# Optimization experiments

Measured on AMD Instinct MI355X. Metric: run time of the kernel, lower is better.

Reference implementation:

```python
import jax, jax.numpy as jnp
import numpy as np

TEMPERATURE = 0.07
EPS = 1e-8  # F.cosine_similarity eps


def setup_inputs() -> dict:
    key = jax.random.key(0)
    k1, k2, k3, k4 = jax.random.split(key, 4)
    N, D, M, C = 4096, 1024, 8192, 100
    q = jax.random.normal(k1, (N, D), dtype=jnp.float32)
    labels = jax.random.randint(k2, (N,), 0, C, dtype=jnp.int32)
    memory_logits = jax.random.normal(k3, (N, M), dtype=jnp.float32)
    memory_targets = jax.random.bernoulli(k4, 0.5, (N, M)).astype(jnp.float32)
    return {"q": q, "labels": labels, "memory_logits": memory_logits,
            "memory_targets": memory_targets}


def reference(q, labels, memory_logits, memory_targets):
    N = q.shape[0]
    # cosine similarity as normalize + GEMM (second operand detached, as in torch)
    qn = q / jnp.maximum(jnp.linalg.norm(q, axis=-1, keepdims=True), EPS)
    sims = qn @ jax.lax.stop_gradient(qn).T               # [N, N]
    src_contrast = sims / TEMPERATURE
    logits_max = jax.lax.stop_gradient(
        jnp.max(src_contrast, axis=1, keepdims=True))
    src_logits = src_contrast - logits_max                # [N, N]
    # positive-pair mask with self excluded
    src_targets = (labels[:, None] == labels[None, :]).astype(jnp.float32)
    self_mask = 1.0 - jnp.eye(N, dtype=jnp.float32)
    src_targets = src_targets * self_mask
    targets = jnp.concatenate([src_targets, memory_targets], axis=1)  # [N, N+M]
    src_exp_logits = jnp.exp(src_logits) * self_mask
    logits = jnp.concatenate([src_logits, memory_logits], axis=1)     # [N, N+M]
    denom = src_exp_logits.sum(axis=1) + jnp.exp(memory_logits).sum(axis=1)
    log_prob = logits - jnp.log(denom)[:, None]
    mean_log_prob_pos = (targets * log_prob).sum(axis=1) / targets.sum(axis=1)
    return -jnp.mean(mean_log_prob_pos)
```

## Files before the change

### kernel.cpp

```cpp
#include <hip/hip_runtime.h>
#include <hip/hip_bf16.h>
#include <math.h>

typedef unsigned short u16;
typedef __bf16 bf16x8 __attribute__((ext_vector_type(8)));
typedef float f32x4 __attribute__((ext_vector_type(4)));
typedef unsigned short u16x4 __attribute__((ext_vector_type(4)));

#define NROW 4096
#define KDIM 1024
#define MDIM 8192
#define TILE 128
#define BK 64
#define NCT (NROW / TILE)
#define NGEMM (NCT * (NROW / TILE))
#define NMEM  NROW

__device__ __forceinline__ u16 f2bf(float x) {
    unsigned int u = __float_as_uint(x);
    unsigned int r = (u + 0x7fffu + ((u >> 16) & 1u)) >> 16;
    return (u16)r;
}

__device__ __forceinline__ void gload16(const u16* g, u16* l) {
    __builtin_amdgcn_global_load_lds(
        (const __attribute__((address_space(1))) void*)g,
        (__attribute__((address_space(3))) void*)l,
        16, 0, 0);
}

__global__ void k_normalize(const float* __restrict__ q, u16* __restrict__ qn) {
    const int r = blockIdx.x;
    const int t = threadIdx.x;
    const int lane = t & 63, wid = t >> 6;
    const float4* qr = (const float4*)(q + (size_t)r * KDIM);
    float4 v = qr[t];
    float ss = v.x * v.x + v.y * v.y + v.z * v.z + v.w * v.w;
    #pragma unroll
    for (int d = 1; d < 64; d <<= 1) ss += __shfl_xor(ss, d);
    __shared__ float red[4];
    if (lane == 0) red[wid] = ss;
    __syncthreads();
    float tot = red[0] + red[1] + red[2] + red[3];
    float nrm = sqrtf(tot);
    float inv = 1.0f / fmaxf(nrm, 1e-8f);
    u16x4 o;
    o[0] = f2bf(v.x * inv); o[1] = f2bf(v.y * inv);
    o[2] = f2bf(v.z * inv); o[3] = f2bf(v.w * inv);
    *(u16x4*)(qn + (size_t)r * KDIM + t * 4) = o;
}

__global__ void k_fused(const u16* __restrict__ qn, const int* __restrict__ labels,
                        const float* __restrict__ ml, const float* __restrict__ mt,
                        float4* __restrict__ partials, float4* __restrict__ memq) {
    __shared__ u16 ldsA[TILE * BK];
    __shared__ u16 ldsB[TILE * BK];
    __shared__ int labR[TILE], labC[TILE];

    const int bid = blockIdx.x;
    const int t = threadIdx.x;
    const int w = t >> 6, lane = t & 63;
    const int g = bid / 5, rem = bid % 5;

    if (rem != 4) {
        const int r = g * 4 + rem;
        const float4* pl = (const float4*)(ml + (size_t)r * MDIM);
        const float4* pt = (const float4*)(mt + (size_t)r * MDIM);
        const int base = w * 512 + lane;
        float4 L[8], T[8];
        #pragma unroll
        for (int j = 0; j < 8; ++j) L[j] = pl[base + j * 64];
        #pragma unroll
        for (int j = 0; j < 8; ++j) T[j] = pt[base + j * 64];
        float S2 = 0.f, dot = 0.f, smt = 0.f;
        #pragma unroll
        for (int j = 0; j < 8; ++j) {
            S2  += __expf(L[j].x) + __expf(L[j].y) + __expf(L[j].z) + __expf(L[j].w);
            dot += T[j].x * L[j].x + T[j].y * L[j].y + T[j].z * L[j].z + T[j].w * L[j].w;
            smt += T[j].x + T[j].y + T[j].z + T[j].w;
        }
        #pragma unroll
        for (int d = 1; d < 64; d <<= 1) {
            S2  += __shfl_xor(S2, d);
            dot += __shfl_xor(dot, d);
            smt += __shfl_xor(smt, d);
        }
        if (lane == 0) memq[r * 4 + w] = make_float4(S2, dot, smt, 0.f);
        return;
    }

    const int ct = g & 31, bi = g >> 5;
    const int rowbase = bi * TILE, colbase = ct * TILE;

    if (t < 128) labR[t] = labels[rowbase + t];
    else labC[t - 128] = labels[colbase + (t - 128)];

    const int wr = (w >> 1) * 64, wc = (w & 1) * 64;
    const int cl = lane & 15, cg = lane >> 4;

    const int sr = lane >> 3;
    const int skb = lane & 7;

    f32x4 acc[4][4];
    #pragma unroll
    for (int i = 0; i < 4; ++i)
        #pragma unroll
        for (int j = 0; j < 4; ++j)
            acc[i][j] = {0.f, 0.f, 0.f, 0.f};

    for (int ks = 0; ks < KDIM / BK; ++ks) {
        const int k0 = ks * BK;
        #pragma unroll
        for (int it = 0; it < 4; ++it) {
            int c = w * 4 + it;
            int rr = c * 8 + sr;
            const u16* ga = qn + (size_t)(rowbase + rr) * KDIM + k0 + skb * 8;
            gload16(ga, ldsA + c * 512);
            const u16* gb = qn + (size_t)(colbase + rr) * KDIM + k0 + skb * 8;
            gload16(gb, ldsB + c * 512);
        }
        asm volatile("s_waitcnt vmcnt(0)" ::: "memory");
        __syncthreads();
        #pragma unroll
        for (int k2 = 0; k2 < 2; ++k2) {
            bf16x8 a[4], b[4];
            #pragma unroll
            for (int f = 0; f < 4; ++f) {
                a[f] = *(const bf16x8*)&ldsA[(wr + f * 16 + cl) * BK + k2 * 32 + cg * 8];
                b[f] = *(const bf16x8*)&ldsB[(wc + f * 16 + cl) * BK + k2 * 32 + cg * 8];
            }
            #pragma unroll
            for (int fm = 0; fm < 4; ++fm)
                #pragma unroll
                for (int fn = 0; fn < 4; ++fn)
                    acc[fm][fn] = __builtin_amdgcn_mfma_f32_16x16x32_bf16(
                        a[fm], b[fn], acc[fm][fn], 0, 0, 0);
        }
        __syncthreads();
    }

    const float invT = (float)(1.0 / 0.07);
    #pragma unroll
    for (int fm = 0; fm < 4; ++fm) {
        #pragma unroll
        for (int reg = 0; reg < 4; ++reg) {
            const int lr = wr + fm * 16 + cg * 4 + reg;
            const int gi = rowbase + lr;
            const int li = labR[lr];
            float c0 = acc[fm][0][reg] * invT;
            float c1 = acc[fm][1][reg] * invT;
            float c2 = acc[fm][2][reg] * invT;
            float c3 = acc[fm][3][reg] * invT;
            float m = fmaxf(fmaxf(c0, c1), fmaxf(c2, c3));
            #pragma unroll
            for (int d = 1; d < 16; d <<= 1) m = fmaxf(m, __shfl_xor(m, d));
            float se = 0.f, ps = 0.f, cnt = 0.f;
            #pragma unroll
            for (int fn = 0; fn < 4; ++fn) {
                float c = (fn == 0) ? c0 : (fn == 1) ? c1 : (fn == 2) ? c2 : c3;
                const int lc = wc + fn * 16 + cl;
                const int gj = colbase + lc;
                const bool self = (gj == gi);
                se += self ? 0.f : __expf(c - m);
                const bool pos = (!self) && (labC[lc] == li);
                ps += pos ? c : 0.f;
                cnt += pos ? 1.f : 0.f;
            }
            #pragma unroll
            for (int d = 1; d < 16; d <<= 1) {
                se  += __shfl_xor(se, d);
                ps  += __shfl_xor(ps, d);
                cnt += __shfl_xor(cnt, d);
            }
            if (cl == 0) partials[(size_t)ct * NROW + gi] = make_float4(m, se, ps, cnt);
        }
    }
}

__global__ void k_combine(const float4* __restrict__ partials, const float4* __restrict__ memq,
                          float* __restrict__ vals) {
    const int r = blockIdx.x * blockDim.x + threadIdx.x;
    if (r >= NROW) return;
    float M = -3.4e38f;
    #pragma unroll 4
    for (int ct = 0; ct < NCT; ++ct) M = fmaxf(M, partials[(size_t)ct * NROW + r].x);
    float S1 = 0.f, ps = 0.f, cnt = 0.f;
    #pragma unroll 4
    for (int ct = 0; ct < NCT; ++ct) {
        float4 p = partials[(size_t)ct * NROW + r];
        S1 += p.y * __expf(p.x - M);
        ps += p.z;
        cnt += p.w;
    }
    float S2 = 0.f, mdot = 0.f, smt = 0.f;
    #pragma unroll
    for (int k = 0; k < 4; ++k) {
        float4 mq = memq[r * 4 + k];
        S2 += mq.x; mdot += mq.y; smt += mq.z;
    }
    float L = logf(S1 + S2);
    float val = (ps - cnt * (M + L) + mdot - smt * L) / (cnt + smt);
    vals[r] = val;
}

__global__ void k_finalize(const float* __restrict__ vals, float* __restrict__ out) {
    const int t = threadIdx.x;
    const int lane = t & 63, wid = t >> 6;
    float s = 0.f;
    for (int i = t; i < NROW; i += 256) s += vals[i];
    #pragma unroll
    for (int d = 1; d < 64; d <<= 1) s += __shfl_xor(s, d);
    __shared__ float red[4];
    if (lane == 0) red[wid] = s;
    __syncthreads();
    if (t == 0) out[0] = -(red[0] + red[1] + red[2] + red[3]) * (1.0f / (float)NROW);
}

extern "C" void kernel_launch(void* const* d_in, const int* in_sizes, int n_in,
                              void* d_out, int out_size, void* d_ws, size_t ws_size,
                              hipStream_t stream) {
    const float* q  = (const float*)d_in[0];
    const int* labels = (const int*)d_in[1];
    const float* ml = (const float*)d_in[2];
    const float* mt = (const float*)d_in[3];
    float* out = (float*)d_out;

    char* w = (char*)d_ws;
    u16* qn          = (u16*)w;
    float4* partials = (float4*)(w + 8388608);
    float4* memq     = (float4*)(w + 10485760);
    float* vals      = (float*)(w + 10747904);

    k_normalize<<<NROW, 256, 0, stream>>>(q, qn);
    k_fused<<<NGEMM + NMEM, 256, 0, stream>>>(qn, labels, ml, mt, partials, memq);
    k_combine<<<NROW / 256, 256, 0, stream>>>(partials, memq, vals);
    k_finalize<<<1, 256, 0, stream>>>(vals, out);
}
```

Baseline: 123.0 us.

## Stream memory rows per wave via double-buffered LDS loads, interleave 1:1 with GEMM

The memory-logit reduction drops from four blocks per row group to 1024 blocks, with each wave now owning a whole row. Each wave streams its row in 1 KB chunks through double-buffered LDS using global_load_lds. Stream blocks now alternate 1:1 with GEMM tiles instead of four stream blocks per GEMM tile. The combine kernel reads one memq entry per row instead of summing four. The aim is to cut block count and register pressure and to overlap streaming with the GEMM tiles. The cost is fewer loads in flight per wave, which may lower achieved bandwidth.

```diff
diff --git a/kernel.cpp b/kernel.cpp
--- a/kernel.cpp
+++ b/kernel.cpp
@@ -14,7 +14,7 @@
 #define BK 64
 #define NCT (NROW / TILE)
 #define NGEMM (NCT * (NROW / TILE))
-#define NMEM  NROW
+#define NSTREAM 1024
 
 __device__ __forceinline__ u16 f2bf(float x) {
     unsigned int u = __float_as_uint(x);
@@ -23,6 +23,13 @@
 }
 
 __device__ __forceinline__ void gload16(const u16* g, u16* l) {
+    __builtin_amdgcn_global_load_lds(
+        (const __attribute__((address_space(1))) void*)g,
+        (__attribute__((address_space(3))) void*)l,
+        16, 0, 0);
+}
+
+__device__ __forceinline__ void gload16f(const float* g, float* l) {
     __builtin_amdgcn_global_load_lds(
         (const __attribute__((address_space(1))) void*)g,
         (__attribute__((address_space(3))) void*)l,
@@ -60,24 +67,48 @@
     const int bid = blockIdx.x;
     const int t = threadIdx.x;
     const int w = t >> 6, lane = t & 63;
-    const int g = bid / 5, rem = bid % 5;
-
-    if (rem != 4) {
-        const int r = g * 4 + rem;
-        const float4* pl = (const float4*)(ml + (size_t)r * MDIM);
-        const float4* pt = (const float4*)(mt + (size_t)r * MDIM);
-        const int base = w * 512 + lane;
-        float4 L[8], T[8];
-        #pragma unroll
-        for (int j = 0; j < 8; ++j) L[j] = pl[base + j * 64];
-        #pragma unroll
-        for (int j = 0; j < 8; ++j) T[j] = pt[base + j * 64];
+    const int sel = (bid >> 1) & 1;
+    const int idx = ((bid >> 2) << 1) | (bid & 1);
+
+    if (sel) {
+        const int r = idx * 4 + w;
+        const float* Lrow = ml + (size_t)r * MDIM;
+        const float* Trow = mt + (size_t)r * MDIM;
+        float* wbase = (float*)((char*)ldsA + w * 4096);
+        float* mlb0 = wbase;
+        float* mlb1 = wbase + 256;
+        float* mtb0 = wbase + 512;
+        float* mtb1 = wbase + 768;
+        const int lo = lane * 4;
+
+        gload16f(Lrow + lo, mlb0);
+        gload16f(Trow + lo, mtb0);
         float S2 = 0.f, dot = 0.f, smt = 0.f;
-        #pragma unroll
-        for (int j = 0; j < 8; ++j) {
-            S2  += __expf(L[j].x) + __expf(L[j].y) + __expf(L[j].z) + __expf(L[j].w);
-            dot += T[j].x * L[j].x + T[j].y * L[j].y + T[j].z * L[j].z + T[j].w * L[j].w;
-            smt += T[j].x + T[j].y + T[j].z + T[j].w;
+        for (int c = 0; c < 32; c += 2) {
+            gload16f(Lrow + (c + 1) * 256 + lo, mlb1);
+            gload16f(Trow + (c + 1) * 256 + lo, mtb1);
+            asm volatile("s_waitcnt vmcnt(2)" ::: "memory");
+            {
+                float4 Lv = ((const float4*)mlb0)[lane];
+                float4 Tv = ((const float4*)mtb0)[lane];
+                S2  += __expf(Lv.x) + __expf(Lv.y) + __expf(Lv.z) + __expf(Lv.w);
+                dot += Tv.x * Lv.x + Tv.y * Lv.y + Tv.z * Lv.z + Tv.w * Lv.w;
+                smt += Tv.x + Tv.y + Tv.z + Tv.w;
+            }
+            if (c + 2 < 32) {
+                gload16f(Lrow + (c + 2) * 256 + lo, mlb0);
+                gload16f(Trow + (c + 2) * 256 + lo, mtb0);
+                asm volatile("s_waitcnt vmcnt(2)" ::: "memory");
+            } else {
+                asm volatile("s_waitcnt vmcnt(0)" ::: "memory");
+            }
+            {
+                float4 Lv = ((const float4*)mlb1)[lane];
+                float4 Tv = ((const float4*)mtb1)[lane];
+                S2  += __expf(Lv.x) + __expf(Lv.y) + __expf(Lv.z) + __expf(Lv.w);
+                dot += Tv.x * Lv.x + Tv.y * Lv.y + Tv.z * Lv.z + Tv.w * Lv.w;
+                smt += Tv.x + Tv.y + Tv.z + Tv.w;
+            }
         }
         #pragma unroll
         for (int d = 1; d < 64; d <<= 1) {
@@ -85,11 +116,11 @@
             dot += __shfl_xor(dot, d);
             smt += __shfl_xor(smt, d);
         }
-        if (lane == 0) memq[r * 4 + w] = make_float4(S2, dot, smt, 0.f);
+        if (lane == 0) memq[r] = make_float4(S2, dot, smt, 0.f);
         return;
     }
 
-    const int ct = g & 31, bi = g >> 5;
+    const int ct = idx & 31, bi = idx >> 5;
     const int rowbase = bi * TILE, colbase = ct * TILE;
 
     if (t < 128) labR[t] = labels[rowbase + t];
@@ -192,14 +223,9 @@
         ps += p.z;
         cnt += p.w;
     }
-    float S2 = 0.f, mdot = 0.f, smt = 0.f;
-    #pragma unroll
-    for (int k = 0; k < 4; ++k) {
-        float4 mq = memq[r * 4 + k];
-        S2 += mq.x; mdot += mq.y; smt += mq.z;
-    }
-    float L = logf(S1 + S2);
-    float val = (ps - cnt * (M + L) + mdot - smt * L) / (cnt + smt);
+    float4 mq = memq[r];
+    float L = logf(S1 + mq.x);
+    float val = (ps - cnt * (M + L) + mq.y - mq.z * L) / (cnt + mq.z);
     vals[r] = val;
 }
 
@@ -229,10 +255,10 @@
     u16* qn          = (u16*)w;
     float4* partials = (float4*)(w + 8388608);
     float4* memq     = (float4*)(w + 10485760);
-    float* vals      = (float*)(w + 10747904);
+    float* vals      = (float*)(w + 10551296);
 
     k_normalize<<<NROW, 256, 0, stream>>>(q, qn);
-    k_fused<<<NGEMM + NMEM, 256, 0, stream>>>(qn, labels, ml, mt, partials, memq);
+    k_fused<<<NGEMM + NSTREAM, 256, 0, stream>>>(qn, labels, ml, mt, partials, memq);
     k_combine<<<NROW / 256, 256, 0, stream>>>(partials, memq, vals);
     k_finalize<<<1, 256, 0, stream>>>(vals, out);
 }
```

After: 122.7 us. No clear change (-0.2%).
